# Kernel optimization log

Measured on AMD Instinct MI355X. Metric: run time of the kernel, lower is better.

Reference implementation:

```python
import jax, jax.numpy as jnp
import numpy as np

D = 2  # spatial dimension


def conv_contract(x, filt, k_in, k_out):
    """Equivariant convolve-then-contract for one (in,out) type pair.
    x: (B, Cin, H, W) + (D,)*k_in
    filt: (O, Cin, 3, 3) + (D,)*k_in + (D,)*k_out
    The first k_in tensor indices of the filter contract with the image's
    tensor indices (absorbed into the conv's input-feature dimension).
    Torus (periodic) padding, stride 1, as per padding='TORUS'.
    """
    B, Cin, H, W = x.shape[0], x.shape[1], x.shape[2], x.shape[3]
    O = filt.shape[0]
    din, dout = D ** k_in, D ** k_out
    # fold tensor-in components into input channels: (B, Cin*din, H, W)
    xr = jnp.moveaxis(x.reshape(B, Cin, H, W, din), -1, 2).reshape(B, Cin * din, H, W)
    # filter -> (O*dout, Cin*din, 3, 3) with matching (Cin, din) ordering
    fr = filt.reshape(O, Cin, 3, 3, din, dout)
    fr = jnp.transpose(fr, (0, 5, 1, 4, 2, 3)).reshape(O * dout, Cin * din, 3, 3)
    # periodic padding then VALID conv == TORUS padding
    xp = jnp.pad(xr, ((0, 0), (0, 0), (1, 1), (1, 1)), mode='wrap')
    out = jax.lax.conv_general_dilated(xp, fr, (1, 1), 'VALID',
                                       dimension_numbers=('NCHW', 'OIHW', 'NCHW'))
    out = jnp.moveaxis(out.reshape(B, O, dout, H, W), 2, -1)  # (B,O,H,W,dout)
    return out.reshape((B, O, H, W) + (D,) * k_out)


def setup_inputs() -> dict:
    key = jax.random.key(0)
    ks = jax.random.split(key, 11)
    B, Cin, Cout, H, W = 8, 96, 96, 128, 128
    N0, N1, N2 = 3, 4, 5  # num invariant filters for tensor order 0,1,2
    b0 = 1.0 / np.sqrt(Cin * 9)
    b1 = 1.0 / np.sqrt(Cin * 9 * D)
    inp = {
        'x_scalar': jax.random.normal(ks[0], (B, Cin, H, W), dtype=jnp.float32),
        'x_vector': jax.random.normal(ks[1], (B, Cin, H, W, D), dtype=jnp.float32),
        'f_k0': jax.random.normal(ks[2], (N0, 3, 3), dtype=jnp.float32),
        'f_k1': jax.random.normal(ks[3], (N1, 3, 3, D), dtype=jnp.float32),
        'f_k2': jax.random.normal(ks[4], (N2, 3, 3, D, D), dtype=jnp.float32),
        'w_ss': jax.random.uniform(ks[5], (Cout, Cin, N0), minval=-b0, maxval=b0),
        'w_sv': jax.random.uniform(ks[6], (Cout, Cin, N1), minval=-b0, maxval=b0),
        'w_vs': jax.random.uniform(ks[7], (Cout, Cin, N1), minval=-b1, maxval=b1),
        'w_vv': jax.random.uniform(ks[8], (Cout, Cin, N2), minval=-b1, maxval=b1),
        'b_s': jax.random.uniform(ks[9], (Cout, 1, 1), minval=-b0, maxval=b0),
        'b_v': jax.random.uniform(ks[10], (Cout, 1, 1, 1), minval=-b1, maxval=b1),
    }
    return inp


def reference(x_scalar, x_vector, f_k0, f_k1, f_k2, w_ss, w_sv, w_vs, w_vv, b_s, b_v):
    # build per-pair filters: weights (O,I,N) x invariant filters (N, 3,3, D^k...)
    f_k0 = jax.lax.stop_gradient(f_k0)
    f_k1 = jax.lax.stop_gradient(f_k1)
    f_k2 = jax.lax.stop_gradient(f_k2)
    F_ss = jnp.einsum('oin,nhw->oihw', w_ss, f_k0)        # scalar->scalar
    F_sv = jnp.einsum('oin,nhwa->oihwa', w_sv, f_k1)      # scalar->vector
    F_vs = jnp.einsum('oin,nhwa->oihwa', w_vs, f_k1)      # vector->scalar
    F_vv = jnp.einsum('oin,nhwab->oihwab', w_vv, f_k2)    # vector->vector
    # convolve each input type against each output type, contract in-tensor
    # indices, and sum contributions per output type
    out_s = conv_contract(x_scalar, F_ss, 0, 0) + conv_contract(x_vector, F_vs, 1, 0)
    out_v = conv_contract(x_scalar, F_sv, 0, 1) + conv_contract(x_vector, F_vv, 1, 1)
    # use_bias='auto': regular bias for scalars, mean-scaled bias for non-scalars
    out_s = out_s + b_s[None]
    out_v = out_v + b_v[None] * jnp.mean(out_v, axis=(2, 3), keepdims=True)
    return out_s, out_v
```

## Files before the change

kernel.cpp:

```cpp
#include <hip/hip_runtime.h>

#define HWSZ 16384
#define CIN 96
#define ICTOT 288
#define OUT_S_ELEMS (8*96*16384)
#define TILE_USH (ICTOT*32)
#define NTILES 81

typedef __attribute__((ext_vector_type(8))) short bf16x8;
typedef __attribute__((ext_vector_type(4))) float f32x4;

#define VMCNT(n) asm volatile("s_waitcnt vmcnt(" #n ")" ::: "memory")

__device__ __forceinline__ unsigned short f2bf(float f){
  unsigned int u = __float_as_uint(f);
  u += 0x7FFFu + ((u >> 16) & 1u);
  return (unsigned short)(u >> 16);
}

__device__ __forceinline__ void gload16(const unsigned short* g, const unsigned short* l){
  __builtin_amdgcn_global_load_lds(
      (const __attribute__((address_space(1))) unsigned int*)g,
      (__attribute__((address_space(3))) unsigned int*)l, 16, 0, 0);
}

__global__ void pack_w_kernel(const float* __restrict__ w_ss, const float* __restrict__ w_sv,
                              const float* __restrict__ w_vs, const float* __restrict__ w_vv,
                              const float* __restrict__ f_k0, const float* __restrict__ f_k1,
                              const float* __restrict__ f_k2, unsigned short* __restrict__ WbT){
  int idx = blockIdx.x*256 + threadIdx.x;
  if (idx >= NTILES*ICTOT*32) return;
  int j = idx / (ICTOT*32); int rem = idx - j*(ICTOT*32);
  int oc = rem >> 5, cc = rem & 31;
  int tap = j % 9, cch = j / 9;
  int ic = cch*32 + cc;
  float acc = 0.f;
  if (oc < 96){
    int o = oc;
    if (ic < CIN){
      int i = ic;
      for (int n=0;n<3;++n) acc += w_ss[(o*CIN+i)*3+n]*f_k0[n*9+tap];
    } else {
      int v = ic-CIN; int i=v>>1, a=v&1;
      for (int n=0;n<4;++n) acc += w_vs[(o*CIN+i)*4+n]*f_k1[(n*9+tap)*2+a];
    }
  } else {
    int ov = oc-96; int o=ov>>1, c=ov&1;
    if (ic < CIN){
      int i = ic;
      for (int n=0;n<4;++n) acc += w_sv[(o*CIN+i)*4+n]*f_k1[(n*9+tap)*2+c];
    } else {
      int v = ic-CIN; int i=v>>1, a=v&1;
      for (int n=0;n<5;++n) acc += w_vv[(o*CIN+i)*5+n]*f_k2[((n*9+tap)*2+a)*2+c];
    }
  }
  int cc_sw = ((((cc>>3) ^ ((oc>>1)&3)) << 3) | (cc & 7));
  WbT[(size_t)j*TILE_USH + oc*32 + cc_sw] = f2bf(acc);
}

__global__ void pack_x_kernel(const float* __restrict__ xs, const float* __restrict__ xv,
                              unsigned short* __restrict__ Xp, float* __restrict__ Part){
  __shared__ float2 tile[32][65];
  __shared__ float red[2][8][32];
  int bid0 = blockIdx.x;
  int t = threadIdx.x;
  if (bid0 < 6144){
    int bid = bid0;
    int ct = bid % 3; int pt = (bid/3) & 255; int b = bid / 768;
    int p0 = pt*64, c0 = ct*32;
    float* tf = (float*)tile;
    int cl = t >> 6, pl = t & 63;
    for (int kk=0; kk<8; ++kk){
      int c = kk*4 + cl;
      tf[c*130 + pl] = xs[(size_t)(b*CIN + c0 + c)*HWSZ + p0 + pl];
    }
    __syncthreads();
    int c = t & 31, pw = t >> 5;
    float psum = 0.f;
    for (int j=0;j<8;++j){
      int p = pw*8 + j;
      float v = tf[c*130 + p];
      psum += v;
      Xp[(size_t)(b*HWSZ + p0 + p)*ICTOT + c0 + c] = f2bf(v);
    }
    red[0][pw][c] = psum;
    __syncthreads();
    if (t < 32){
      float s = 0.f;
      #pragma unroll
      for (int k=0;k<8;++k) s += red[0][k][t];
      Part[((size_t)b*ICTOT + c0 + t)*256 + pt] = s;
    }
  } else {
    int bid = bid0 - 6144;
    int ct = bid % 3; int pt = (bid/3) & 255; int b = bid / 768;
    int p0 = pt*64, c0 = ct*32;
    int cl = t >> 6, pl = t & 63;
    const float2* src = (const float2*)xv;
    for (int kk=0; kk<8; ++kk){
      int c = kk*4 + cl;
      tile[c][pl] = src[(size_t)(b*CIN + c0 + c)*HWSZ + p0 + pl];
    }
    __syncthreads();
    int c = t & 31, pw = t >> 5;
    float sx = 0.f, sy = 0.f;
    for (int j=0;j<8;++j){
      int p = pw*8 + j;
      float2 v = tile[c][p];
      sx += v.x; sy += v.y;
      unsigned int u = (unsigned int)f2bf(v.x) | ((unsigned int)f2bf(v.y) << 16);
      *(unsigned int*)&Xp[(size_t)(b*HWSZ + p0 + p)*ICTOT + CIN + 2*(c0+c)] = u;
    }
    red[0][pw][c] = sx; red[1][pw][c] = sy;
    __syncthreads();
    if (t < 32){
      float s0 = 0.f, s1 = 0.f;
      #pragma unroll
      for (int k=0;k<8;++k){ s0 += red[0][k][t]; s1 += red[1][k][t]; }
      Part[((size_t)b*ICTOT + CIN + 2*(c0+t)    )*256 + pt] = s0;
      Part[((size_t)b*ICTOT + CIN + 2*(c0+t) + 1)*256 + pt] = s1;
    }
  }
}

__global__ void reduce_part_kernel(const float* __restrict__ Part, float* __restrict__ Ssum){
  int b = blockIdx.x;
  int t = threadIdx.x;
  if (t >= ICTOT) return;
  const float* p = Part + ((size_t)b*ICTOT + t)*256;
  float s = 0.f;
  #pragma unroll 8
  for (int i=0;i<256;++i) s += p[i];
  Ssum[b*ICTOT + t] = s;
}

__global__ void mbias_kernel(const float* __restrict__ w_sv, const float* __restrict__ w_vv,
                             const float* __restrict__ f_k1, const float* __restrict__ f_k2,
                             const float* __restrict__ b_v, const float* __restrict__ Ssum,
                             float* __restrict__ MB){
  int row = blockIdx.x;
  int o = row >> 1, c = row & 1;
  int lane = threadIdx.x;
  float f1s[4], f2s[5][2];
  for (int n=0;n<4;++n){
    float s=0.f;
    for (int tap=0;tap<9;++tap) s += f_k1[(n*9+tap)*2+c];
    f1s[n]=s;
  }
  for (int n=0;n<5;++n)
    for (int a=0;a<2;++a){
      float s=0.f;
      for (int tap=0;tap<9;++tap) s += f_k2[((n*9+tap)*2+a)*2+c];
      f2s[n][a]=s;
    }
  float wv[5];
  for (int k=0;k<5;++k){
    int ic = lane + 64*k;
    float v = 0.f;
    if (ic < CIN){
      for (int n=0;n<4;++n) v += w_sv[(o*CIN+ic)*4+n]*f1s[n];
    } else if (ic < ICTOT){
      int u = ic-CIN; int i=u>>1, a=u&1;
      for (int n=0;n<5;++n) v += w_vv[(o*CIN+i)*5+n]*f2s[n][a];
    }
    wv[k] = v;
  }
  for (int b=0;b<8;++b){
    float acc = 0.f;
    for (int k=0;k<5;++k){
      int ic = lane + 64*k;
      if (ic < ICTOT) acc += wv[k]*Ssum[b*ICTOT+ic];
    }
    for (int m=1;m<64;m<<=1) acc += __shfl_xor(acc, m);
    if (lane == 0) MB[b*192+row] = b_v[o]*acc*(1.f/16384.f);
  }
}

__global__ __launch_bounds__(512,2) void conv_mfma_kernel(
    const unsigned short* __restrict__ Xp, const unsigned short* __restrict__ WbT,
    const float* __restrict__ b_s, const float* __restrict__ MB,
    float* __restrict__ out){
  __shared__ unsigned short Ash[3][1536*8];
  __shared__ unsigned short Bsh[2][2048*8];

  int bid = blockIdx.x;
  int b = bid & 7, rp = bid >> 3;
  int tid = threadIdx.x;
  int lane = tid & 63, w = tid >> 6;
  int wr = w >> 2, wc = w & 3;
  int cl = lane & 15, g = lane >> 4;

  f32x4 acc[9][4];
  #pragma unroll
  for (int m=0;m<9;++m)
    #pragma unroll
    for (int n=0;n<4;++n) acc[m][n] = (f32x4){0.f,0.f,0.f,0.f};

  const size_t xb = (size_t)b * HWSZ * ICTOT;
  const unsigned short* srcB[4];
  #pragma unroll
  for (int i=0;i<4;++i){
    int f = i*512 + tid;
    int j = f >> 9, px = (f >> 2) & 127, cp = f & 3;
    int cps = cp ^ ((px >> 1) & 3);
    int hs = (2*rp - 1 + j + 128) & 127;
    srcB[i] = Xp + xb + ((size_t)(hs*128 + px))*ICTOT + cps*8;
  }
  const unsigned short* srcA = WbT + tid*8;
  const int wlds = w*64*8;
  const int Abase = (wr*144 + cl)*32 + ((g ^ ((cl>>1)&3))*8);
  const int pxb = (wc & 1)*64 + cl;
  const int jr0 = (wc >> 1);

  int boff[3][4];
  #pragma unroll
  for (int kx=0;kx<3;++kx)
    #pragma unroll
    for (int n=0;n<4;++n){
      int px = (pxb + n*16 + kx + 127) & 127;
      boff[kx][n] = px*32 + ((g ^ ((px >> 1) & 3))*8);
    }

  #pragma unroll
  for (int i=0;i<4;++i) gload16(srcB[i], &Bsh[0][i*4096 + wlds]);
  #pragma unroll
  for (int i=0;i<3;++i) gload16(srcA + 0*TILE_USH + i*4096, &Ash[0][i*4096 + wlds]);
  #pragma unroll
  for (int i=0;i<3;++i) gload16(srcA + 1*TILE_USH + i*4096, &Ash[1][i*4096 + wlds]);
  VMCNT(0);
  __builtin_amdgcn_s_barrier();

  bf16x8 afc[9], bfc[4];
  #pragma unroll
  for (int n=0;n<4;++n) bfc[n] = *(const bf16x8*)&Bsh[0][jr0*4096 + boff[0][n]];
  #pragma unroll
  for (int m=0;m<9;++m) afc[m] = *(const bf16x8*)&Ash[0][Abase + m*512];

  const unsigned short* cA = srcA;
  for (int c = 0; c < 9; ++c){
    const unsigned short* Bcur = Bsh[c & 1];
    unsigned short* Bnxt = (unsigned short*)Bsh[(c & 1) ^ 1];
    #pragma unroll
    for (int t = 0; t < 9; ++t){
      if (c < 8 || t <= 6){
        #pragma unroll
        for (int i=0;i<3;++i)
          gload16(cA + (t+2)*TILE_USH + i*4096, &Ash[(t+2)%3][i*4096 + wlds]);
      }
      if (t == 0 && c < 8){
        #pragma unroll
        for (int i=0;i<4;++i)
          gload16(srcB[i] + (c+1)*32, &Bnxt[i*4096 + wlds]);
      }
      __builtin_amdgcn_s_setprio(1);
      #pragma unroll
      for (int m=0;m<9;++m){
        #pragma unroll
        for (int n=0;n<4;++n)
          acc[m][n] = __builtin_amdgcn_mfma_f32_16x16x32_bf16(afc[m], bfc[n], acc[m][n], 0,0,0);
      }
      __builtin_amdgcn_s_setprio(0);
      if (c < 8){ if (t <= 1) { VMCNT(7); } else { VMCNT(3); } }
      else      { if (t <= 6) { VMCNT(3); } else if (t == 7) { VMCNT(0); } }
      if (c < 8 || t < 8){
        const int tau = (t+1)%9;
        const int ky = tau/3, kx = tau%3;
        const unsigned short* Bsrc = (t < 8 ? Bcur : (const unsigned short*)Bnxt) + (jr0 + ky)*4096;
        #pragma unroll
        for (int n=0;n<4;++n) bfc[n] = *(const bf16x8*)&Bsrc[boff[kx][n]];
        const unsigned short* At = Ash[(t+1)%3];
        #pragma unroll
        for (int m=0;m<9;++m) afc[m] = *(const bf16x8*)&At[Abase + m*512];
      }
      __builtin_amdgcn_sched_barrier(0);
      __builtin_amdgcn_s_barrier();
    }
    cA += 9*TILE_USH;
  }

  const int orow = 2*rp + (wc >> 1);
  const int colb = (wc & 1)*64;
  #pragma unroll
  for (int m=0;m<9;++m){
    int ocb = wr*144 + m*16 + 4*g;
    if (wr == 0 && m < 6){
      #pragma unroll
      for (int r=0;r<4;++r){
        int oc = ocb + r;
        float bias = b_s[oc];
        #pragma unroll
        for (int n=0;n<4;++n){
          int p = orow*128 + colb + n*16 + cl;
          out[(size_t)(b*96+oc)*HWSZ + p] = acc[m][n][r] + bias;
        }
      }
    } else {
      float2* outv = (float2*)(out + OUT_S_ELEMS);
      int row0 = ocb - 96;
      int o0 = row0 >> 1;
      float mb0 = MB[b*192+row0  ], mb1 = MB[b*192+row0+1];
      float mb2 = MB[b*192+row0+2], mb3 = MB[b*192+row0+3];
      #pragma unroll
      for (int n=0;n<4;++n){
        int p = orow*128 + colb + n*16 + cl;
        outv[(size_t)(b*96+o0  )*HWSZ + p] = (float2){acc[m][n][0]+mb0, acc[m][n][1]+mb1};
        outv[(size_t)(b*96+o0+1)*HWSZ + p] = (float2){acc[m][n][2]+mb2, acc[m][n][3]+mb3};
      }
    }
  }
}

extern "C" void kernel_launch(void* const* d_in, const int* in_sizes, int n_in,
                              void* d_out, int out_size, void* d_ws, size_t ws_size,
                              hipStream_t stream){
  const float* xs   = (const float*)d_in[0];
  const float* xv   = (const float*)d_in[1];
  const float* f_k0 = (const float*)d_in[2];
  const float* f_k1 = (const float*)d_in[3];
  const float* f_k2 = (const float*)d_in[4];
  const float* w_ss = (const float*)d_in[5];
  const float* w_sv = (const float*)d_in[6];
  const float* w_vs = (const float*)d_in[7];
  const float* w_vv = (const float*)d_in[8];
  const float* b_s  = (const float*)d_in[9];
  const float* b_v  = (const float*)d_in[10];
  float* out = (float*)d_out;

  char* ws = (char*)d_ws;
  unsigned short* WbT = (unsigned short*)ws;
  const size_t XP_OFF = (size_t)NTILES*TILE_USH*2 + 6144;
  unsigned short* Xp = (unsigned short*)(ws + XP_OFF);
  const size_t PART_OFF = XP_OFF + (size_t)8*HWSZ*ICTOT*2;
  float* Part = (float*)(ws + PART_OFF);
  float* Ssum = (float*)(ws + PART_OFF + 2359296);
  float* MB   = (float*)(ws + PART_OFF + 2359296 + 9216);

  pack_w_kernel<<<(NTILES*ICTOT*32 + 255)/256, 256, 0, stream>>>(
      w_ss, w_sv, w_vs, w_vv, f_k0, f_k1, f_k2, WbT);
  pack_x_kernel<<<12288, 256, 0, stream>>>(xs, xv, Xp, Part);
  reduce_part_kernel<<<8, 320, 0, stream>>>(Part, Ssum);
  mbias_kernel<<<192, 64, 0, stream>>>(w_sv, w_vv, f_k1, f_k2, b_v, Ssum, MB);
  conv_mfma_kernel<<<512, 512, 0, stream>>>(Xp, WbT, b_s, MB, out);
}
```

Measured before the change: 240.0 us.

## Interleave LDS fragment loads with MFMAs and trim oversized weight-tile copies

The main loop body moves into a templated per-chunk routine. Reads of the next step's A fragments are now interleaved with the MFMA issue, and B fragments are double-buffered in registers, so LDS latency can hide behind matrix math. Weight-tile copies are cut from three 4096-element loads to exactly the 9216-element tile, which removes redundant global traffic and shrinks the A buffers. In exchange, every step now does a full vmcnt(0) wait at its start, so less global prefetch stays in flight. LDS reads also happen before the barrier that would guarantee other waves' async copies have landed, which risks a data race.

```diff
diff --git a/kernel.cpp b/kernel.cpp
--- a/kernel.cpp
+++ b/kernel.cpp
@@ -176,12 +176,70 @@
   }
 }
 
+template<bool LASTC>
+__device__ __forceinline__ void do_chunk(int c,
+    const unsigned short* __restrict__ WbT,
+    unsigned short* Ash0,
+    const unsigned short* Bcur, unsigned short* Bnxt,
+    const unsigned short* const (&srcB)[4],
+    int tid, int w, int jr0, int Abase, const int (&boff)[12],
+    bf16x8 (&afc)[9], bf16x8 (&bfcA)[4], bf16x8 (&bfcB)[4],
+    f32x4 (&acc)[9][4])
+{
+  const unsigned short* cA = WbT + (size_t)(9*c)*TILE_USH;
+  const int wl = w*512;
+  #pragma unroll
+  for (int t=0;t<9;++t){
+    VMCNT(0);
+    if (!LASTC && t==0){
+      #pragma unroll
+      for (int i=0;i<4;++i) gload16(srcB[i] + (c+1)*32, Bnxt + i*4096 + wl);
+    }
+    if (!LASTC || t<=6){
+      const unsigned short* s = cA + (size_t)(t+2)*TILE_USH;
+      unsigned short* d = Ash0 + ((t+2)%3)*9216;
+      gload16(s + tid*8,            d + wl);
+      gload16(s + (512+tid)*8,      d + 4096 + wl);
+      if (tid < 128) gload16(s + (1024+tid)*8, d + 8192 + wl);
+    }
+    const int tau = (t+1)%9;
+    const int ky = tau/3, kx = tau%3;
+    const unsigned short* Asrc = Ash0 + ((t+1)%3)*9216;
+    const unsigned short* Bsrc = (t<8 ? Bcur : (const unsigned short*)Bnxt) + (jr0+ky)*4096;
+    if (!LASTC || t<8){
+      if ((t & 1) == 0){
+        #pragma unroll
+        for (int n=0;n<4;++n) bfcB[n] = *(const bf16x8*)&Bsrc[boff[kx*4+n]];
+      } else {
+        #pragma unroll
+        for (int n=0;n<4;++n) bfcA[n] = *(const bf16x8*)&Bsrc[boff[kx*4+n]];
+      }
+    }
+    __builtin_amdgcn_s_setprio(1);
+    #pragma unroll
+    for (int m=0;m<9;++m){
+      #pragma unroll
+      for (int n=0;n<4;++n){
+        const bf16x8 bop = ((t & 1) == 0) ? bfcA[n] : bfcB[n];
+        acc[m][n] = __builtin_amdgcn_mfma_f32_16x16x32_bf16(afc[m], bop, acc[m][n], 0,0,0);
+      }
+      if (!LASTC || t<8) afc[m] = *(const bf16x8*)&Asrc[Abase + m*512];
+    }
+    __builtin_amdgcn_s_setprio(0);
+    __builtin_amdgcn_s_barrier();
+  }
+  if (!LASTC){
+    #pragma unroll
+    for (int n=0;n<4;++n) bfcA[n] = bfcB[n];
+  }
+}
+
 __global__ __launch_bounds__(512,2) void conv_mfma_kernel(
     const unsigned short* __restrict__ Xp, const unsigned short* __restrict__ WbT,
     const float* __restrict__ b_s, const float* __restrict__ MB,
     float* __restrict__ out){
-  __shared__ unsigned short Ash[3][1536*8];
-  __shared__ unsigned short Bsh[2][2048*8];
+  __shared__ unsigned short Ash[3][9216];
+  __shared__ unsigned short Bsh[2][16384];
 
   int bid = blockIdx.x;
   int b = bid & 7, rp = bid >> 3;
@@ -206,77 +264,45 @@
     int hs = (2*rp - 1 + j + 128) & 127;
     srcB[i] = Xp + xb + ((size_t)(hs*128 + px))*ICTOT + cps*8;
   }
-  const unsigned short* srcA = WbT + tid*8;
-  const int wlds = w*64*8;
+  const int wl = w*512;
   const int Abase = (wr*144 + cl)*32 + ((g ^ ((cl>>1)&3))*8);
   const int pxb = (wc & 1)*64 + cl;
   const int jr0 = (wc >> 1);
 
-  int boff[3][4];
+  int boff[12];
   #pragma unroll
   for (int kx=0;kx<3;++kx)
     #pragma unroll
     for (int n=0;n<4;++n){
       int px = (pxb + n*16 + kx + 127) & 127;
-      boff[kx][n] = px*32 + ((g ^ ((px >> 1) & 3))*8);
-    }
-
-  #pragma unroll
-  for (int i=0;i<4;++i) gload16(srcB[i], &Bsh[0][i*4096 + wlds]);
-  #pragma unroll
-  for (int i=0;i<3;++i) gload16(srcA + 0*TILE_USH + i*4096, &Ash[0][i*4096 + wlds]);
-  #pragma unroll
-  for (int i=0;i<3;++i) gload16(srcA + 1*TILE_USH + i*4096, &Ash[1][i*4096 + wlds]);
+      boff[kx*4+n] = px*32 + ((g ^ ((px >> 1) & 3))*8);
+    }
+
+  #pragma unroll
+  for (int i=0;i<4;++i) gload16(srcB[i], &Bsh[0][i*4096 + wl]);
+  #pragma unroll
+  for (int j=0;j<2;++j){
+    const unsigned short* s = WbT + (size_t)j*TILE_USH;
+    unsigned short* d = &Ash[j][0];
+    gload16(s + tid*8,            d + wl);
+    gload16(s + (512+tid)*8,      d + 4096 + wl);
+    if (tid < 128) gload16(s + (1024+tid)*8, d + 8192 + wl);
+  }
   VMCNT(0);
   __builtin_amdgcn_s_barrier();
 
-  bf16x8 afc[9], bfc[4];
-  #pragma unroll
-  for (int n=0;n<4;++n) bfc[n] = *(const bf16x8*)&Bsh[0][jr0*4096 + boff[0][n]];
+  bf16x8 afc[9], bfcA[4], bfcB[4];
+  #pragma unroll
+  for (int n=0;n<4;++n) bfcA[n] = *(const bf16x8*)&Bsh[0][jr0*4096 + boff[n]];
   #pragma unroll
   for (int m=0;m<9;++m) afc[m] = *(const bf16x8*)&Ash[0][Abase + m*512];
 
-  const unsigned short* cA = srcA;
-  for (int c = 0; c < 9; ++c){
-    const unsigned short* Bcur = Bsh[c & 1];
-    unsigned short* Bnxt = (unsigned short*)Bsh[(c & 1) ^ 1];
-    #pragma unroll
-    for (int t = 0; t < 9; ++t){
-      if (c < 8 || t <= 6){
-        #pragma unroll
-        for (int i=0;i<3;++i)
-          gload16(cA + (t+2)*TILE_USH + i*4096, &Ash[(t+2)%3][i*4096 + wlds]);
-      }
-      if (t == 0 && c < 8){
-        #pragma unroll
-        for (int i=0;i<4;++i)
-          gload16(srcB[i] + (c+1)*32, &Bnxt[i*4096 + wlds]);
-      }
-      __builtin_amdgcn_s_setprio(1);
-      #pragma unroll
-      for (int m=0;m<9;++m){
-        #pragma unroll
-        for (int n=0;n<4;++n)
-          acc[m][n] = __builtin_amdgcn_mfma_f32_16x16x32_bf16(afc[m], bfc[n], acc[m][n], 0,0,0);
-      }
-      __builtin_amdgcn_s_setprio(0);
-      if (c < 8){ if (t <= 1) { VMCNT(7); } else { VMCNT(3); } }
-      else      { if (t <= 6) { VMCNT(3); } else if (t == 7) { VMCNT(0); } }
-      if (c < 8 || t < 8){
-        const int tau = (t+1)%9;
-        const int ky = tau/3, kx = tau%3;
-        const unsigned short* Bsrc = (t < 8 ? Bcur : (const unsigned short*)Bnxt) + (jr0 + ky)*4096;
-        #pragma unroll
-        for (int n=0;n<4;++n) bfc[n] = *(const bf16x8*)&Bsrc[boff[kx][n]];
-        const unsigned short* At = Ash[(t+1)%3];
-        #pragma unroll
-        for (int m=0;m<9;++m) afc[m] = *(const bf16x8*)&At[Abase + m*512];
-      }
-      __builtin_amdgcn_sched_barrier(0);
-      __builtin_amdgcn_s_barrier();
-    }
-    cA += 9*TILE_USH;
-  }
+  for (int c=0;c<8;++c){
+    do_chunk<false>(c, WbT, &Ash[0][0], &Bsh[c&1][0], &Bsh[(c&1)^1][0],
+                    srcB, tid, w, jr0, Abase, boff, afc, bfcA, bfcB, acc);
+  }
+  do_chunk<true>(8, WbT, &Ash[0][0], &Bsh[0][0], &Bsh[1][0],
+                 srcB, tid, w, jr0, Abase, boff, afc, bfcA, bfcB, acc);
 
   const int orow = 2*rp + (wc >> 1);
   const int colb = (wc & 1)*64;
```

Measured after the change: 402.0 us. +67.5%, slower.
